# Kernel optimization log

Measured on AMD Instinct MI355X. Metric: run time of the kernel, lower is better.

Reference implementation:

```python
import jax, jax.numpy as jnp
import numpy as np

D_MODEL = 1024
NUM_HEADS = 16
D_K = D_MODEL // NUM_HEADS


def setup_inputs() -> dict:
    key = jax.random.key(0)
    ks = jax.random.split(key, 11)
    B, S = 2, 2048
    scale = 1.0 / np.sqrt(D_MODEL)
    return {
        "Q": jax.random.normal(ks[0], (B, S, D_MODEL), jnp.float32),
        "K": jax.random.normal(ks[1], (B, S, D_MODEL), jnp.float32),
        "V": jax.random.normal(ks[2], (B, S, D_MODEL), jnp.float32),
        "Wq": jax.random.normal(ks[3], (D_MODEL, D_MODEL), jnp.float32) * scale,
        "bq": jnp.zeros((D_MODEL,), jnp.float32),
        "Wk": jax.random.normal(ks[4], (D_MODEL, D_MODEL), jnp.float32) * scale,
        "bk": jnp.zeros((D_MODEL,), jnp.float32),
        "Wv": jax.random.normal(ks[5], (D_MODEL, D_MODEL), jnp.float32) * scale,
        "bv": jnp.zeros((D_MODEL,), jnp.float32),
        "Wo": jax.random.normal(ks[6], (D_MODEL, D_MODEL), jnp.float32) * scale,
        "bo": jnp.zeros((D_MODEL,), jnp.float32),
    }


def reference(Q, K, V, Wq, bq, Wk, bk, Wv, bv, Wo, bo):
    B, S, _ = Q.shape
    # linear projections (torch Linear: x @ W.T + b)
    q = Q @ Wq.T + bq
    k = K @ Wk.T + bk
    v = V @ Wv.T + bv
    # split heads: [B, S, H, d_k] -> [B, H, S, d_k]
    q = q.reshape(B, S, NUM_HEADS, D_K).transpose(0, 2, 1, 3)
    k = k.reshape(B, S, NUM_HEADS, D_K).transpose(0, 2, 1, 3)
    v = v.reshape(B, S, NUM_HEADS, D_K).transpose(0, 2, 1, 3)
    # scaled dot-product attention, full [B, H, S, S] scores as in original
    scores = jnp.einsum("bhqd,bhkd->bhqk", q, k) / jnp.sqrt(jnp.float32(D_K))
    probs = jax.nn.softmax(scores, axis=-1)
    attn = jnp.einsum("bhqk,bhkd->bhqd", probs, v)
    # merge heads and output projection
    attn = attn.transpose(0, 2, 1, 3).reshape(B, S, D_MODEL)
    return attn @ Wo.T + bo
```

## Files before the change

kernel.cpp:

```cpp
#include <hip/hip_runtime.h>
#include <cstdint>
#include <cstddef>

#define D_MODEL 1024
#define NHEADS 16
#define DK 64
#define BATCH 2
#define SEQ 2048
#define MROWS 4096

using f32x4 = __attribute__((ext_vector_type(4))) float;
using f32x16 = __attribute__((ext_vector_type(16))) float;
using u16x8 = __attribute__((ext_vector_type(8))) unsigned short;
using u32x4 = __attribute__((ext_vector_type(4))) unsigned int;
using bf16x8 = __attribute__((ext_vector_type(8))) __bf16;

static __device__ __forceinline__ f32x4 mfma16(u16x8 a, u16x8 b, f32x4 c) {
    return __builtin_amdgcn_mfma_f32_16x16x32_bf16(
        __builtin_bit_cast(bf16x8, a), __builtin_bit_cast(bf16x8, b), c, 0, 0, 0);
}
static __device__ __forceinline__ f32x16 mfma32(u16x8 a, u16x8 b, f32x16 c) {
    return __builtin_amdgcn_mfma_f32_32x32x16_bf16(
        __builtin_bit_cast(bf16x8, a), __builtin_bit_cast(bf16x8, b), c, 0, 0, 0);
}

static __device__ __forceinline__ unsigned short f2b(float f) {
    unsigned int u = __float_as_uint(f);
    u += 0x7fffu + ((u >> 16) & 1u);
    return (unsigned short)(u >> 16);
}
static __device__ __forceinline__ unsigned int cvt_pk(float lo, float hi) {
    unsigned int r;
    asm("v_cvt_pk_bf16_f32 %0, %1, %2" : "=v"(r) : "v"(lo), "v"(hi));
    return r;
}
static __device__ __forceinline__ void plswap(unsigned int& a, unsigned int& b) {
    asm("v_permlane32_swap_b32 %0, %1" : "+v"(a), "+v"(b));
}
static __device__ __forceinline__ float fexp2(float x) {
#if __has_builtin(__builtin_amdgcn_exp2f)
    return __builtin_amdgcn_exp2f(x);
#else
    float r;
    asm("v_exp_f32 %0, %1" : "=v"(r) : "v"(x));
    return r;
#endif
}
static __device__ __forceinline__ void gll16(const void* g, void* l) {
    __builtin_amdgcn_global_load_lds(
        (const __attribute__((address_space(1))) void*)g,
        (__attribute__((address_space(3))) void*)l, 16, 0, 0);
}
#define SBAR() __builtin_amdgcn_s_barrier()
#define SCHED0() __builtin_amdgcn_sched_barrier(0)

__global__ __launch_bounds__(256) void cvtw_kernel(const float* __restrict__ w0,
                                                   const float* __restrict__ w1,
                                                   const float* __restrict__ w2,
                                                   const float* __restrict__ w3,
                                                   unsigned short* __restrict__ out,
                                                   int n4, float scale0) {
    const float* srcs[4] = {w0, w1, w2, w3};
    const float* src = srcs[blockIdx.y];
    unsigned short* dst = out + (size_t)blockIdx.y * (size_t)n4 * 4;
    float scale = (blockIdx.y == 0) ? scale0 : 1.0f;
    int i = blockIdx.x * 256 + threadIdx.x;
    if (i < n4) {
        float4 v = reinterpret_cast<const float4*>(src)[i];
        ushort4 o;
        o.x = f2b(v.x * scale);
        o.y = f2b(v.y * scale);
        o.z = f2b(v.z * scale);
        o.w = f2b(v.w * scale);
        reinterpret_cast<ushort4*>(dst)[i] = o;
    }
}

__global__ __launch_bounds__(256) void cvta_kernel(const float* __restrict__ a0,
                                                   const float* __restrict__ a1,
                                                   const float* __restrict__ a2,
                                                   unsigned short* __restrict__ out,
                                                   int n4) {
    const float* srcs[3] = {a0, a1, a2};
    const float* src = srcs[blockIdx.y];
    unsigned short* dst = out + (size_t)blockIdx.y * (size_t)n4 * 4;
    int i = blockIdx.x * 256 + threadIdx.x;
    if (i < n4) {
        float4 v = reinterpret_cast<const float4*>(src)[i];
        ushort4 o;
        o.x = f2b(v.x);
        o.y = f2b(v.y);
        o.z = f2b(v.z);
        o.w = f2b(v.w);
        reinterpret_cast<ushort4*>(dst)[i] = o;
    }
}

__global__ __launch_bounds__(256, 2) void gemm_qkv_kernel(
    const unsigned short* __restrict__ Abf,
    const unsigned short* __restrict__ W,
    unsigned short* __restrict__ qo, unsigned short* __restrict__ ko,
    unsigned short* __restrict__ vto,
    const float* __restrict__ b0, const float* __restrict__ b1, const float* __restrict__ b2,
    float qsc) {
    __shared__ __align__(16) char Ab[2][16384];
    __shared__ __align__(16) char Wb[2][16384];

    const int tid = threadIdx.x;
    const int lane = tid & 63;
    const int wid = tid >> 6;
    const int wr = wid >> 1, wc = wid & 1;
    const int g = (lane >> 4) & 3, l16 = lane & 15;

    const int logical = ((int)blockIdx.x & 7) * 96 + ((int)blockIdx.x >> 3);
    const int m = logical >> 8;
    const int rem = logical & 255;
    const int y = rem >> 3, xc = rem & 7;
    const int row0 = y * 128;
    const int arow0 = m * MROWS + row0;
    const int wrow0 = m * 1024 + xc * 128;

    const int srow = wid * 8 + (lane >> 3);
    const int g16 = (lane & 7) ^ (lane >> 3);

    auto stage = [&](int k0, int buf) {
#pragma unroll
        for (int pp = 0; pp < 4; ++pp) {
            const char* s = (const char*)Abf + (size_t)(arow0 + pp * 32 + srow) * 2048 + k0 * 2 + g16 * 16;
            gll16(s, Ab[buf] + pp * 4096 + wid * 1024);
        }
#pragma unroll
        for (int pp = 0; pp < 4; ++pp) {
            const char* s = (const char*)W + (size_t)(wrow0 + pp * 32 + srow) * 2048 + k0 * 2 + g16 * 16;
            gll16(s, Wb[buf] + pp * 4096 + wid * 1024);
        }
    };

    f32x4 acc[4][4] = {};
    stage(0, 0);

    const int swz = (l16 & 7) << 4;
    for (int t = 0; t < 16; ++t) {
        if (t < 15) stage((t + 1) * 64, (t & 1) ^ 1);
        if (t < 15) asm volatile("s_waitcnt vmcnt(8)" ::: "memory");
        else asm volatile("s_waitcnt vmcnt(0)" ::: "memory");
        SCHED0();
        SBAR();
        SCHED0();
#pragma unroll
        for (int kk = 0; kk < 2; ++kk) {
            const int sw0 = (kk * 64 + g * 16) ^ swz;
            u16x8 af[4], bf[4];
#pragma unroll
            for (int mi = 0; mi < 4; ++mi)
                af[mi] = *reinterpret_cast<const u16x8*>(Ab[t & 1] + (wr * 64 + mi * 16 + l16) * 128 + sw0);
#pragma unroll
            for (int ni = 0; ni < 4; ++ni)
                bf[ni] = *reinterpret_cast<const u16x8*>(Wb[t & 1] + (wc * 64 + ni * 16 + l16) * 128 + sw0);
            __builtin_amdgcn_s_setprio(1);
#pragma unroll
            for (int mi = 0; mi < 4; ++mi)
#pragma unroll
                for (int ni = 0; ni < 4; ++ni)
                    acc[mi][ni] = mfma16(af[mi], bf[ni], acc[mi][ni]);
            __builtin_amdgcn_s_setprio(0);
        }
        SBAR();
        SCHED0();
    }

    const float* bias = (m == 0) ? b0 : ((m == 1) ? b1 : b2);
    const float bsc = (m == 0) ? qsc : 1.0f;
#pragma unroll
    for (int mi = 0; mi < 4; ++mi) {
#pragma unroll
        for (int ni = 0; ni < 4; ++ni) {
            int r = row0 + wr * 64 + mi * 16 + g * 4;
            int cl = xc * 128 + wc * 64 + ni * 16 + l16;
            float bv = bsc * bias[cl];
            if (m < 2) {
                unsigned short* outp = m ? ko : qo;
#pragma unroll
                for (int j = 0; j < 4; ++j)
                    outp[(size_t)(r + j) * 1024 + cl] = f2b(acc[mi][ni][j] + bv);
            } else {
                ushort4 o;
                o.x = f2b(acc[mi][ni][0] + bv);
                o.y = f2b(acc[mi][ni][1] + bv);
                o.z = f2b(acc[mi][ni][2] + bv);
                o.w = f2b(acc[mi][ni][3] + bv);
                *reinterpret_cast<ushort4*>(vto + (size_t)cl * MROWS + r) = o;
            }
        }
    }
}

__global__ __launch_bounds__(256, 2) void gemm_out_kernel(
    const unsigned short* __restrict__ Abf,
    const unsigned short* __restrict__ W,
    float* __restrict__ fo,
    const float* __restrict__ bias) {
    __shared__ __align__(16) char Ab[2][16384];
    __shared__ __align__(16) char Wb[2][16384];

    const int tid = threadIdx.x;
    const int lane = tid & 63;
    const int wid = tid >> 6;
    const int wr = wid >> 1, wc = wid & 1;
    const int g = (lane >> 4) & 3, l16 = lane & 15;

    const int logical = ((int)blockIdx.x & 7) * 32 + ((int)blockIdx.x >> 3);
    const int y = logical >> 3, xc = logical & 7;
    const int row0 = y * 128;
    const int wrow0 = xc * 128;

    const int srow = wid * 8 + (lane >> 3);
    const int g16 = (lane & 7) ^ (lane >> 3);

    auto stage = [&](int k0, int buf) {
#pragma unroll
        for (int pp = 0; pp < 4; ++pp) {
            const char* s = (const char*)Abf + (size_t)(row0 + pp * 32 + srow) * 2048 + k0 * 2 + g16 * 16;
            gll16(s, Ab[buf] + pp * 4096 + wid * 1024);
        }
#pragma unroll
        for (int pp = 0; pp < 4; ++pp) {
            const char* s = (const char*)W + (size_t)(wrow0 + pp * 32 + srow) * 2048 + k0 * 2 + g16 * 16;
            gll16(s, Wb[buf] + pp * 4096 + wid * 1024);
        }
    };

    f32x4 acc[4][4] = {};
    stage(0, 0);

    const int swz = (l16 & 7) << 4;
    for (int t = 0; t < 16; ++t) {
        if (t < 15) stage((t + 1) * 64, (t & 1) ^ 1);
        if (t < 15) asm volatile("s_waitcnt vmcnt(8)" ::: "memory");
        else asm volatile("s_waitcnt vmcnt(0)" ::: "memory");
        SCHED0();
        SBAR();
        SCHED0();
#pragma unroll
        for (int kk = 0; kk < 2; ++kk) {
            const int sw0 = (kk * 64 + g * 16) ^ swz;
            u16x8 af[4], bf[4];
#pragma unroll
            for (int mi = 0; mi < 4; ++mi)
                af[mi] = *reinterpret_cast<const u16x8*>(Ab[t & 1] + (wr * 64 + mi * 16 + l16) * 128 + sw0);
#pragma unroll
            for (int ni = 0; ni < 4; ++ni)
                bf[ni] = *reinterpret_cast<const u16x8*>(Wb[t & 1] + (wc * 64 + ni * 16 + l16) * 128 + sw0);
            __builtin_amdgcn_s_setprio(1);
#pragma unroll
            for (int mi = 0; mi < 4; ++mi)
#pragma unroll
                for (int ni = 0; ni < 4; ++ni)
                    acc[mi][ni] = mfma16(af[mi], bf[ni], acc[mi][ni]);
            __builtin_amdgcn_s_setprio(0);
        }
        SBAR();
        SCHED0();
    }

#pragma unroll
    for (int mi = 0; mi < 4; ++mi) {
#pragma unroll
        for (int ni = 0; ni < 4; ++ni) {
            int r = row0 + wr * 64 + mi * 16 + g * 4;
            int cl = xc * 128 + wc * 64 + ni * 16 + l16;
            float bv = bias[cl];
#pragma unroll
            for (int j = 0; j < 4; ++j)
                fo[(size_t)(r + j) * 1024 + cl] = acc[mi][ni][j] + bv;
        }
    }
}

__global__ __launch_bounds__(512, 2) void attn_kernel(
    const unsigned short* __restrict__ qp,
    const unsigned short* __restrict__ kp,
    const unsigned short* __restrict__ vT,
    unsigned short* __restrict__ ao) {
    __shared__ __align__(16) char lds[65536];

    const int tid = threadIdx.x;
    const int lane = tid & 63;
    const int wid = tid >> 6;
    const int wq = wid & 3, wk = wid >> 2;
    const int l31 = lane & 31, hi = lane >> 5;

    const int logical = ((int)blockIdx.x & 7) * 64 + ((int)blockIdx.x >> 3);
    const int qt = logical & 15;
    const int bh = logical >> 4;
    const int b = bh >> 4, h = bh & 15;
    const int ch = h * DK;
    const int q0 = b * SEQ + qt * 128;

    const int srow = wid * 8 + (lane >> 3);
    const int g16 = (lane & 7) ^ (lane >> 3);
    const char* kbase = (const char*)kp + ((size_t)(b * SEQ + srow)) * 2048 + ch * 2 + g16 * 16;
    const char* vbase = (const char*)vT + ((size_t)(ch + srow)) * (MROWS * 2) + (size_t)b * SEQ * 2 + g16 * 16;

    const char* qr = (const char*)qp + (size_t)(q0 + wq * 32 + l31) * 2048 + ch * 2;
    u16x8 qf[4];
#pragma unroll
    for (int t = 0; t < 4; ++t)
        qf[t] = *reinterpret_cast<const u16x8*>(qr + t * 32 + hi * 16);

    auto stageKV = [&](int kt2, char* base) {
        gll16(kbase + (size_t)kt2 * (64 * 2048), base + wid * 1024);
        gll16(kbase + (size_t)(kt2 * 64 + 1024) * 2048, base + 8192 + wid * 1024);
        gll16(vbase + kt2 * 128, base + 16384 + wid * 1024);
        gll16(vbase + kt2 * 128 + 2048, base + 24576 + wid * 1024);
    };

    const int swz = (lane & 7) << 4;
    f32x16 acco[2] = {};
    float l0 = 0.f, l1 = 0.f, l2 = 0.f, l3 = 0.f;

    stageKV(0, lds);
    for (int kt = 0; kt < 16; ++kt) {
        if (kt < 15) stageKV(kt + 1, lds + (((kt + 1) & 1) << 15));
        if (kt < 15) asm volatile("s_waitcnt vmcnt(4)" ::: "memory");
        else asm volatile("s_waitcnt vmcnt(0)" ::: "memory");
        SCHED0();
        SBAR();
        SCHED0();
        const char* cb = lds + ((kt & 1) << 15);
        const char* Kb = cb + wk * 8192;
        const char* Vb = cb + 16384 + wk * 8192;

        unsigned int pf[4][4];
#pragma unroll
        for (int ts = 0; ts < 2; ++ts) {
            f32x16 s = {};
            __builtin_amdgcn_s_setprio(1);
#pragma unroll
            for (int t = 0; t < 4; ++t) {
                u16x8 kf = *reinterpret_cast<const u16x8*>(Kb + (ts * 32 + l31) * 128 + ((32 * t + 16 * hi) ^ swz));
                s = mfma32(kf, qf[t], s);
            }
            __builtin_amdgcn_s_setprio(0);
            float p[16];
#pragma unroll
            for (int r = 0; r < 16; r += 4) {
                p[r] = fexp2(s[r]);
                p[r + 1] = fexp2(s[r + 1]);
                p[r + 2] = fexp2(s[r + 2]);
                p[r + 3] = fexp2(s[r + 3]);
                l0 += p[r];
                l1 += p[r + 1];
                l2 += p[r + 2];
                l3 += p[r + 3];
            }
#pragma unroll
            for (int i = 0; i < 2; ++i) {
                unsigned int a = cvt_pk(p[2 * i], p[2 * i + 1]);
                unsigned int bb = cvt_pk(p[4 + 2 * i], p[5 + 2 * i]);
                plswap(a, bb);
                pf[2 * ts][i] = a;
                pf[2 * ts][i + 2] = bb;
                unsigned int a2 = cvt_pk(p[8 + 2 * i], p[9 + 2 * i]);
                unsigned int b2 = cvt_pk(p[12 + 2 * i], p[13 + 2 * i]);
                plswap(a2, b2);
                pf[2 * ts + 1][i] = a2;
                pf[2 * ts + 1][i + 2] = b2;
            }
        }
        __builtin_amdgcn_s_setprio(1);
#pragma unroll
        for (int t = 0; t < 4; ++t) {
            u32x4 wv = {pf[t][0], pf[t][1], pf[t][2], pf[t][3]};
            u16x8 pfr = __builtin_bit_cast(u16x8, wv);
#pragma unroll
            for (int dt = 0; dt < 2; ++dt) {
                u16x8 vf = *reinterpret_cast<const u16x8*>(Vb + (dt * 32 + l31) * 128 + ((32 * t + 16 * hi) ^ swz));
                acco[dt] = mfma32(vf, pfr, acco[dt]);
            }
        }
        __builtin_amdgcn_s_setprio(0);
        SBAR();
        SCHED0();
    }

    float L = (l0 + l1) + (l2 + l3);

    float Lh = L + __shfl_xor(L, 32);
    float* cmb = reinterpret_cast<float*>(lds);
    float* slot = cmb + (size_t)tid * 18;
    f32x16 outg = acco[1 ^ wk];
#pragma unroll
    for (int mm = 0; mm < 8; ++mm)
        *reinterpret_cast<float2*>(slot + 2 * mm) = float2{outg[2 * mm], outg[2 * mm + 1]};
    slot[16] = Lh;
    __syncthreads();
    const float* ps = cmb + (size_t)(tid ^ 256) * 18;
    f32x16 kept = acco[wk];
#pragma unroll
    for (int mm = 0; mm < 8; ++mm) {
        float2 t2 = *reinterpret_cast<const float2*>(ps + 2 * mm);
        kept[2 * mm] += t2.x;
        kept[2 * mm + 1] += t2.y;
    }
    float rl = 1.0f / (Lh + ps[16]);
    __syncthreads();

    char* ot = lds + wid * 2304;
    const int r7 = l31 & 7;
#pragma unroll
    for (int mm = 0; mm < 4; ++mm) {
        uint2 pko;
        pko.x = cvt_pk(kept[4 * mm] * rl, kept[4 * mm + 1] * rl);
        pko.y = cvt_pk(kept[4 * mm + 2] * rl, kept[4 * mm + 3] * rl);
        *reinterpret_cast<uint2*>(ot + l31 * 72 + (((2 * mm + hi) ^ r7) << 3)) = pko;
    }
    const int rr = lane >> 1, half = lane & 1;
    const int rb7 = rr & 7;
    uint2 t0 = *reinterpret_cast<const uint2*>(ot + rr * 72 + (((half * 4 + 0) ^ rb7) << 3));
    uint2 t1 = *reinterpret_cast<const uint2*>(ot + rr * 72 + (((half * 4 + 1) ^ rb7) << 3));
    uint2 t2 = *reinterpret_cast<const uint2*>(ot + rr * 72 + (((half * 4 + 2) ^ rb7) << 3));
    uint2 t3 = *reinterpret_cast<const uint2*>(ot + rr * 72 + (((half * 4 + 3) ^ rb7) << 3));
    unsigned short* dst = ao + (size_t)(q0 + wq * 32 + rr) * 1024 + ch + wk * 32 + half * 16;
    uint4 o0 = {t0.x, t0.y, t1.x, t1.y};
    uint4 o1 = {t2.x, t2.y, t3.x, t3.y};
    *reinterpret_cast<uint4*>(dst) = o0;
    *reinterpret_cast<uint4*>(dst + 8) = o1;
}

extern "C" void kernel_launch(void* const* d_in, const int* in_sizes, int n_in,
                              void* d_out, int out_size, void* d_ws, size_t ws_size,
                              hipStream_t stream) {
    const float* Q = (const float*)d_in[0];
    const float* K = (const float*)d_in[1];
    const float* V = (const float*)d_in[2];
    const float* Wq = (const float*)d_in[3];
    const float* bq = (const float*)d_in[4];
    const float* Wk = (const float*)d_in[5];
    const float* bk = (const float*)d_in[6];
    const float* Wv = (const float*)d_in[7];
    const float* bv = (const float*)d_in[8];
    const float* Wo = (const float*)d_in[9];
    const float* bo = (const float*)d_in[10];

    unsigned short* ws = (unsigned short*)d_ws;
    const size_t SZ = (size_t)MROWS * D_MODEL;
    const size_t WSZ = (size_t)D_MODEL * D_MODEL;
    unsigned short* bufW = ws;
    unsigned short* abf = bufW + 4 * WSZ;
    unsigned short* qp = abf + 3 * SZ;
    unsigned short* kp = qp + SZ;
    unsigned short* vT = kp + SZ;
    unsigned short* ao = vT + SZ;

    const float qscale = 0.125f * 1.44269504088896f;

    dim3 blk(256);
    dim3 gcw((unsigned)(WSZ / 4 / 256), 4);
    cvtw_kernel<<<gcw, blk, 0, stream>>>(Wq, Wk, Wv, Wo, bufW, (int)(WSZ / 4), qscale);
    dim3 gca((unsigned)(SZ / 4 / 256), 3);
    cvta_kernel<<<gca, blk, 0, stream>>>(Q, K, V, abf, (int)(SZ / 4));

    gemm_qkv_kernel<<<dim3(768), blk, 0, stream>>>(abf, bufW, qp, kp, vT, bq, bk, bv, qscale);

    attn_kernel<<<dim3(512), dim3(512), 0, stream>>>(qp, kp, vT, ao);

    gemm_out_kernel<<<dim3(256), blk, 0, stream>>>(ao, bufW + 3 * WSZ, (float*)d_out, bo);
}
```

Baseline: 135.0 us.

## Halve LDS tile depth in GEMMs and attention to raise occupancy

The QKV and output GEMMs now stage K-slices of 32 instead of 64, which halves their LDS buffers and doubles the loop trip count, with a new swizzled staging and read layout. The attention kernel now stages 32 keys per iteration instead of 64, which shrinks LDS from 64KB to 36KB. Launch bounds rise to allow 4 and 8 blocks per CU. The aim is more resident waves to hide memory latency. In exchange there are twice as many barriers and waitcnt points per unit of work, and register pressure is tighter under the higher occupancy bounds.

```diff
diff --git a/kernel.cpp b/kernel.cpp
--- a/kernel.cpp
+++ b/kernel.cpp
@@ -96,15 +96,16 @@
     }
 }
 
-__global__ __launch_bounds__(256, 2) void gemm_qkv_kernel(
+
+__global__ __launch_bounds__(256, 4) void gemm_qkv_kernel(
     const unsigned short* __restrict__ Abf,
     const unsigned short* __restrict__ W,
     unsigned short* __restrict__ qo, unsigned short* __restrict__ ko,
     unsigned short* __restrict__ vto,
     const float* __restrict__ b0, const float* __restrict__ b1, const float* __restrict__ b2,
     float qsc) {
-    __shared__ __align__(16) char Ab[2][16384];
-    __shared__ __align__(16) char Wb[2][16384];
+    __shared__ __align__(16) char Ab[2][8192];
+    __shared__ __align__(16) char Wb[2][8192];
 
     const int tid = threadIdx.x;
     const int lane = tid & 63;
@@ -120,51 +121,48 @@
     const int arow0 = m * MROWS + row0;
     const int wrow0 = m * 1024 + xc * 128;
 
-    const int srow = wid * 8 + (lane >> 3);
-    const int g16 = (lane & 7) ^ (lane >> 3);
+    const int sline = tid >> 3;
+    const int sgl = (tid & 7) ^ (sline & 7);
+    const int srow = sline * 2 + (sgl >> 2);
+    const int skcol = (sgl & 3) * 8;
 
     auto stage = [&](int k0, int buf) {
-#pragma unroll
-        for (int pp = 0; pp < 4; ++pp) {
-            const char* s = (const char*)Abf + (size_t)(arow0 + pp * 32 + srow) * 2048 + k0 * 2 + g16 * 16;
-            gll16(s, Ab[buf] + pp * 4096 + wid * 1024);
-        }
-#pragma unroll
-        for (int pp = 0; pp < 4; ++pp) {
-            const char* s = (const char*)W + (size_t)(wrow0 + pp * 32 + srow) * 2048 + k0 * 2 + g16 * 16;
-            gll16(s, Wb[buf] + pp * 4096 + wid * 1024);
-        }
+        const char* a0 = (const char*)Abf + (size_t)(arow0 + srow) * 2048 + (size_t)(k0 + skcol) * 2;
+        gll16(a0, Ab[buf] + wid * 1024);
+        gll16(a0 + (size_t)64 * 2048, Ab[buf] + 4096 + wid * 1024);
+        const char* w0 = (const char*)W + (size_t)(wrow0 + srow) * 2048 + (size_t)(k0 + skcol) * 2;
+        gll16(w0, Wb[buf] + wid * 1024);
+        gll16(w0 + (size_t)64 * 2048, Wb[buf] + 4096 + wid * 1024);
     };
+
+    const int rswz = ((((l16 & 1) << 2) + g) ^ ((l16 >> 1) & 7)) << 4;
+    const int abase = (wr * 32 + (l16 >> 1)) * 128 + rswz;
+    const int bbase = (wc * 32 + (l16 >> 1)) * 128 + rswz;
 
     f32x4 acc[4][4] = {};
     stage(0, 0);
 
-    const int swz = (l16 & 7) << 4;
-    for (int t = 0; t < 16; ++t) {
-        if (t < 15) stage((t + 1) * 64, (t & 1) ^ 1);
-        if (t < 15) asm volatile("s_waitcnt vmcnt(8)" ::: "memory");
+    for (int t = 0; t < 32; ++t) {
+        if (t < 31) stage((t + 1) * 32, (t & 1) ^ 1);
+        if (t < 31) asm volatile("s_waitcnt vmcnt(4)" ::: "memory");
         else asm volatile("s_waitcnt vmcnt(0)" ::: "memory");
         SCHED0();
         SBAR();
         SCHED0();
-#pragma unroll
-        for (int kk = 0; kk < 2; ++kk) {
-            const int sw0 = (kk * 64 + g * 16) ^ swz;
-            u16x8 af[4], bf[4];
-#pragma unroll
-            for (int mi = 0; mi < 4; ++mi)
-                af[mi] = *reinterpret_cast<const u16x8*>(Ab[t & 1] + (wr * 64 + mi * 16 + l16) * 128 + sw0);
+        u16x8 af[4], bf[4];
+#pragma unroll
+        for (int mi = 0; mi < 4; ++mi)
+            af[mi] = *reinterpret_cast<const u16x8*>(Ab[t & 1] + abase + mi * 1024);
+#pragma unroll
+        for (int ni = 0; ni < 4; ++ni)
+            bf[ni] = *reinterpret_cast<const u16x8*>(Wb[t & 1] + bbase + ni * 1024);
+        __builtin_amdgcn_s_setprio(1);
+#pragma unroll
+        for (int mi = 0; mi < 4; ++mi)
 #pragma unroll
             for (int ni = 0; ni < 4; ++ni)
-                bf[ni] = *reinterpret_cast<const u16x8*>(Wb[t & 1] + (wc * 64 + ni * 16 + l16) * 128 + sw0);
-            __builtin_amdgcn_s_setprio(1);
-#pragma unroll
-            for (int mi = 0; mi < 4; ++mi)
-#pragma unroll
-                for (int ni = 0; ni < 4; ++ni)
-                    acc[mi][ni] = mfma16(af[mi], bf[ni], acc[mi][ni]);
-            __builtin_amdgcn_s_setprio(0);
-        }
+                acc[mi][ni] = mfma16(af[mi], bf[ni], acc[mi][ni]);
+        __builtin_amdgcn_s_setprio(0);
         SBAR();
         SCHED0();
     }
@@ -175,7 +173,7 @@
     for (int mi = 0; mi < 4; ++mi) {
 #pragma unroll
         for (int ni = 0; ni < 4; ++ni) {
-            int r = row0 + wr * 64 + mi * 16 + g * 4;
+            int r = row0 + wr * 64 + mi * 16 + (g & 3) * 4;
             int cl = xc * 128 + wc * 64 + ni * 16 + l16;
             float bv = bsc * bias[cl];
             if (m < 2) {
@@ -195,13 +193,13 @@
     }
 }
 
-__global__ __launch_bounds__(256, 2) void gemm_out_kernel(
+__global__ __launch_bounds__(256, 4) void gemm_out_kernel(
     const unsigned short* __restrict__ Abf,
     const unsigned short* __restrict__ W,
     float* __restrict__ fo,
     const float* __restrict__ bias) {
-    __shared__ __align__(16) char Ab[2][16384];
-    __shared__ __align__(16) char Wb[2][16384];
+    __shared__ __align__(16) char Ab[2][8192];
+    __shared__ __align__(16) char Wb[2][8192];
 
     const int tid = threadIdx.x;
     const int lane = tid & 63;
@@ -214,51 +212,48 @@
     const int row0 = y * 128;
     const int wrow0 = xc * 128;
 
-    const int srow = wid * 8 + (lane >> 3);
-    const int g16 = (lane & 7) ^ (lane >> 3);
+    const int sline = tid >> 3;
+    const int sgl = (tid & 7) ^ (sline & 7);
+    const int srow = sline * 2 + (sgl >> 2);
+    const int skcol = (sgl & 3) * 8;
 
     auto stage = [&](int k0, int buf) {
-#pragma unroll
-        for (int pp = 0; pp < 4; ++pp) {
-            const char* s = (const char*)Abf + (size_t)(row0 + pp * 32 + srow) * 2048 + k0 * 2 + g16 * 16;
-            gll16(s, Ab[buf] + pp * 4096 + wid * 1024);
-        }
-#pragma unroll
-        for (int pp = 0; pp < 4; ++pp) {
-            const char* s = (const char*)W + (size_t)(wrow0 + pp * 32 + srow) * 2048 + k0 * 2 + g16 * 16;
-            gll16(s, Wb[buf] + pp * 4096 + wid * 1024);
-        }
+        const char* a0 = (const char*)Abf + (size_t)(row0 + srow) * 2048 + (size_t)(k0 + skcol) * 2;
+        gll16(a0, Ab[buf] + wid * 1024);
+        gll16(a0 + (size_t)64 * 2048, Ab[buf] + 4096 + wid * 1024);
+        const char* w0 = (const char*)W + (size_t)(wrow0 + srow) * 2048 + (size_t)(k0 + skcol) * 2;
+        gll16(w0, Wb[buf] + wid * 1024);
+        gll16(w0 + (size_t)64 * 2048, Wb[buf] + 4096 + wid * 1024);
     };
+
+    const int rswz = ((((l16 & 1) << 2) + g) ^ ((l16 >> 1) & 7)) << 4;
+    const int abase = (wr * 32 + (l16 >> 1)) * 128 + rswz;
+    const int bbase = (wc * 32 + (l16 >> 1)) * 128 + rswz;
 
     f32x4 acc[4][4] = {};
     stage(0, 0);
 
-    const int swz = (l16 & 7) << 4;
-    for (int t = 0; t < 16; ++t) {
-        if (t < 15) stage((t + 1) * 64, (t & 1) ^ 1);
-        if (t < 15) asm volatile("s_waitcnt vmcnt(8)" ::: "memory");
+    for (int t = 0; t < 32; ++t) {
+        if (t < 31) stage((t + 1) * 32, (t & 1) ^ 1);
+        if (t < 31) asm volatile("s_waitcnt vmcnt(4)" ::: "memory");
         else asm volatile("s_waitcnt vmcnt(0)" ::: "memory");
         SCHED0();
         SBAR();
         SCHED0();
-#pragma unroll
-        for (int kk = 0; kk < 2; ++kk) {
-            const int sw0 = (kk * 64 + g * 16) ^ swz;
-            u16x8 af[4], bf[4];
-#pragma unroll
-            for (int mi = 0; mi < 4; ++mi)
-                af[mi] = *reinterpret_cast<const u16x8*>(Ab[t & 1] + (wr * 64 + mi * 16 + l16) * 128 + sw0);
+        u16x8 af[4], bf[4];
+#pragma unroll
+        for (int mi = 0; mi < 4; ++mi)
+            af[mi] = *reinterpret_cast<const u16x8*>(Ab[t & 1] + abase + mi * 1024);
+#pragma unroll
+        for (int ni = 0; ni < 4; ++ni)
+            bf[ni] = *reinterpret_cast<const u16x8*>(Wb[t & 1] + bbase + ni * 1024);
+        __builtin_amdgcn_s_setprio(1);
+#pragma unroll
+        for (int mi = 0; mi < 4; ++mi)
 #pragma unroll
             for (int ni = 0; ni < 4; ++ni)
-                bf[ni] = *reinterpret_cast<const u16x8*>(Wb[t & 1] + (wc * 64 + ni * 16 + l16) * 128 + sw0);
-            __builtin_amdgcn_s_setprio(1);
-#pragma unroll
-            for (int mi = 0; mi < 4; ++mi)
-#pragma unroll
-                for (int ni = 0; ni < 4; ++ni)
-                    acc[mi][ni] = mfma16(af[mi], bf[ni], acc[mi][ni]);
-            __builtin_amdgcn_s_setprio(0);
-        }
+                acc[mi][ni] = mfma16(af[mi], bf[ni], acc[mi][ni]);
+        __builtin_amdgcn_s_setprio(0);
         SBAR();
         SCHED0();
     }
@@ -277,12 +272,12 @@
     }
 }
 
-__global__ __launch_bounds__(512, 2) void attn_kernel(
+__global__ __launch_bounds__(512, 8) void attn_kernel(
     const unsigned short* __restrict__ qp,
     const unsigned short* __restrict__ kp,
     const unsigned short* __restrict__ vT,
     unsigned short* __restrict__ ao) {
-    __shared__ __align__(16) char lds[65536];
+    __shared__ __align__(16) char lds[36864];
 
     const int tid = threadIdx.x;
     const int lane = tid & 63;
@@ -297,10 +292,14 @@
     const int ch = h * DK;
     const int q0 = b * SEQ + qt * 128;
 
-    const int srow = wid * 8 + (lane >> 3);
-    const int g16 = (lane & 7) ^ (lane >> 3);
-    const char* kbase = (const char*)kp + ((size_t)(b * SEQ + srow)) * 2048 + ch * 2 + g16 * 16;
-    const char* vbase = (const char*)vT + ((size_t)(ch + srow)) * (MROWS * 2) + (size_t)b * SEQ * 2 + g16 * 16;
+    const int kline = tid >> 3;
+    const int kgl = (tid & 7) ^ (kline & 7);
+    const char* ksrc0 = (const char*)kp +
+        ((size_t)(b * SEQ + (kline >> 5) * 1024 + (kline & 31))) * 2048 + ch * 2 + kgl * 16;
+    const int vgl = (tid & 7) ^ ((tid >> 3) & 7);
+    const char* vsrc0 = (const char*)vT +
+        ((size_t)(ch + (tid >> 3))) * (MROWS * 2) +
+        ((size_t)b * SEQ + (vgl >> 2) * 1024 + (vgl & 3) * 8) * 2;
 
     const char* qr = (const char*)qp + (size_t)(q0 + wq * 32 + l31) * 2048 + ch * 2;
     u16x8 qf[4];
@@ -309,73 +308,70 @@
         qf[t] = *reinterpret_cast<const u16x8*>(qr + t * 32 + hi * 16);
 
     auto stageKV = [&](int kt2, char* base) {
-        gll16(kbase + (size_t)kt2 * (64 * 2048), base + wid * 1024);
-        gll16(kbase + (size_t)(kt2 * 64 + 1024) * 2048, base + 8192 + wid * 1024);
-        gll16(vbase + kt2 * 128, base + 16384 + wid * 1024);
-        gll16(vbase + kt2 * 128 + 2048, base + 24576 + wid * 1024);
+        gll16(ksrc0 + (size_t)kt2 * 65536, base + wid * 1024);
+        gll16(vsrc0 + kt2 * 64, base + 8192 + wid * 1024);
     };
 
-    const int swz = (lane & 7) << 4;
+    const int lswz = lane & 7;
     f32x16 acco[2] = {};
     float l0 = 0.f, l1 = 0.f, l2 = 0.f, l3 = 0.f;
 
     stageKV(0, lds);
-    for (int kt = 0; kt < 16; ++kt) {
-        if (kt < 15) stageKV(kt + 1, lds + (((kt + 1) & 1) << 15));
-        if (kt < 15) asm volatile("s_waitcnt vmcnt(4)" ::: "memory");
+    for (int kt = 0; kt < 32; ++kt) {
+        if (kt < 31) stageKV(kt + 1, lds + (((kt + 1) & 1) << 14));
+        if (kt < 31) asm volatile("s_waitcnt vmcnt(2)" ::: "memory");
         else asm volatile("s_waitcnt vmcnt(0)" ::: "memory");
         SCHED0();
         SBAR();
         SCHED0();
-        const char* cb = lds + ((kt & 1) << 15);
-        const char* Kb = cb + wk * 8192;
-        const char* Vb = cb + 16384 + wk * 8192;
-
-        unsigned int pf[4][4];
-#pragma unroll
-        for (int ts = 0; ts < 2; ++ts) {
-            f32x16 s = {};
-            __builtin_amdgcn_s_setprio(1);
-#pragma unroll
-            for (int t = 0; t < 4; ++t) {
-                u16x8 kf = *reinterpret_cast<const u16x8*>(Kb + (ts * 32 + l31) * 128 + ((32 * t + 16 * hi) ^ swz));
-                s = mfma32(kf, qf[t], s);
-            }
-            __builtin_amdgcn_s_setprio(0);
-            float p[16];
-#pragma unroll
-            for (int r = 0; r < 16; r += 4) {
-                p[r] = fexp2(s[r]);
-                p[r + 1] = fexp2(s[r + 1]);
-                p[r + 2] = fexp2(s[r + 2]);
-                p[r + 3] = fexp2(s[r + 3]);
-                l0 += p[r];
-                l1 += p[r + 1];
-                l2 += p[r + 2];
-                l3 += p[r + 3];
-            }
-#pragma unroll
-            for (int i = 0; i < 2; ++i) {
-                unsigned int a = cvt_pk(p[2 * i], p[2 * i + 1]);
-                unsigned int bb = cvt_pk(p[4 + 2 * i], p[5 + 2 * i]);
-                plswap(a, bb);
-                pf[2 * ts][i] = a;
-                pf[2 * ts][i + 2] = bb;
-                unsigned int a2 = cvt_pk(p[8 + 2 * i], p[9 + 2 * i]);
-                unsigned int b2 = cvt_pk(p[12 + 2 * i], p[13 + 2 * i]);
-                plswap(a2, b2);
-                pf[2 * ts + 1][i] = a2;
-                pf[2 * ts + 1][i + 2] = b2;
-            }
-        }
+        const char* cb = lds + ((kt & 1) << 14);
+
+        f32x16 s = {};
         __builtin_amdgcn_s_setprio(1);
 #pragma unroll
         for (int t = 0; t < 4; ++t) {
-            u32x4 wv = {pf[t][0], pf[t][1], pf[t][2], pf[t][3]};
+            u16x8 kf = *reinterpret_cast<const u16x8*>(
+                cb + (wk * 32 + l31) * 128 + (((2 * t + hi) ^ lswz) << 4));
+            s = mfma32(kf, qf[t], s);
+        }
+        __builtin_amdgcn_s_setprio(0);
+
+        float p[16];
+#pragma unroll
+        for (int r = 0; r < 16; r += 4) {
+            p[r] = fexp2(s[r]);
+            p[r + 1] = fexp2(s[r + 1]);
+            p[r + 2] = fexp2(s[r + 2]);
+            p[r + 3] = fexp2(s[r + 3]);
+            l0 += p[r];
+            l1 += p[r + 1];
+            l2 += p[r + 2];
+            l3 += p[r + 3];
+        }
+        unsigned int pf0[4], pf1[4];
+#pragma unroll
+        for (int i = 0; i < 2; ++i) {
+            unsigned int a = cvt_pk(p[2 * i], p[2 * i + 1]);
+            unsigned int bb = cvt_pk(p[4 + 2 * i], p[5 + 2 * i]);
+            plswap(a, bb);
+            pf0[i] = a;
+            pf0[i + 2] = bb;
+            unsigned int a2 = cvt_pk(p[8 + 2 * i], p[9 + 2 * i]);
+            unsigned int b2 = cvt_pk(p[12 + 2 * i], p[13 + 2 * i]);
+            plswap(a2, b2);
+            pf1[i] = a2;
+            pf1[i + 2] = b2;
+        }
+        __builtin_amdgcn_s_setprio(1);
+#pragma unroll
+        for (int t = 0; t < 2; ++t) {
+            u32x4 wv = t ? u32x4{pf1[0], pf1[1], pf1[2], pf1[3]}
+                         : u32x4{pf0[0], pf0[1], pf0[2], pf0[3]};
             u16x8 pfr = __builtin_bit_cast(u16x8, wv);
 #pragma unroll
             for (int dt = 0; dt < 2; ++dt) {
-                u16x8 vf = *reinterpret_cast<const u16x8*>(Vb + (dt * 32 + l31) * 128 + ((32 * t + 16 * hi) ^ swz));
+                u16x8 vf = *reinterpret_cast<const u16x8*>(
+                    cb + 8192 + (dt * 32 + l31) * 128 + ((((wk << 2) + 2 * t + hi) ^ lswz) << 4));
                 acco[dt] = mfma32(vf, pfr, acco[dt]);
             }
         }
```

Result: slower. 242.6 us (+79.7%).
